# Performance work log

Hardware: AMD Instinct MI355X
Metric: run time of the kernel (lower is better)

Reference implementation:

```python
import jax, jax.numpy as jnp
import numpy as np

B, L = 8, 896
D_MODEL, N_HEAD, D_HEAD, D_INNER = 320, 10, 32, 1280
LN_EPS = 1e-5


def layernorm(x, g, b):
    mu = jnp.mean(x, axis=-1, keepdims=True)
    var = jnp.mean(jnp.square(x - mu), axis=-1, keepdims=True)
    return (x - mu) * jax.lax.rsqrt(var + LN_EPS) * g + b


def setup_inputs() -> dict:
    key = jax.random.key(0)
    ks = jax.random.split(key, 8)
    w = lambda k, shape: (jax.random.normal(k, shape, jnp.float32) * 0.02)
    return {
        "Z": jax.random.normal(ks[0], (B, L, D_MODEL), jnp.float32),
        "D": jax.random.uniform(ks[1], (B, L, L), jnp.float32),  # nonneg sq-distance bias
        "new_mask": jnp.zeros((B, L, L), jnp.float32),           # additive mask (0 = keep)
        "mask": jnp.ones((B, L, L), jnp.float32),                # multiplicative validity mask
        "gamma": jnp.ones((4, 4), jnp.float32),
        "w_qkv": w(ks[2], (D_MODEL, 3 * D_MODEL)),
        "b_qkv": jnp.zeros((3 * D_MODEL,), jnp.float32),
        "w_o": w(ks[3], (D_MODEL, D_MODEL)),
        "ln1_g": jnp.ones((D_MODEL,), jnp.float32),
        "ln1_b": jnp.zeros((D_MODEL,), jnp.float32),
        "ln2_g": jnp.ones((D_MODEL,), jnp.float32),
        "ln2_b": jnp.zeros((D_MODEL,), jnp.float32),
        "w1": w(ks[4], (D_MODEL, D_INNER)),
        "b1": jnp.zeros((D_INNER,), jnp.float32),
        "w2": w(ks[5], (D_INNER, D_MODEL)),
        "b2": jnp.zeros((D_MODEL,), jnp.float32),
        "N": 128, "M": 256, "P": 512,
    }


def reference(Z, D, new_mask, mask, gamma, w_qkv, b_qkv, w_o,
              ln1_g, ln1_b, ln2_g, ln2_b, w1, b1, w2, b2, N, M, P):
    bsz, n_elem, _ = Z.shape
    sqrtd = np.sqrt(D_HEAD).astype(np.float32)

    # per-pair type bias: segment ids 0=atom,1=bond,2=triplet (use_quad=False)
    seg = jnp.concatenate([
        jnp.zeros((N,), jnp.int32),
        jnp.ones((M,), jnp.int32),
        jnp.full((P,), 2, jnp.int32),
    ])  # [L]
    gamma_mask = gamma[seg[:, None], seg[None, :]]  # [L, L]

    inp = Z
    Zn = layernorm(Z, ln1_g, ln1_b)
    qkv = (Zn @ w_qkv + b_qkv).reshape(bsz, n_elem, N_HEAD, 3 * D_HEAD)
    Z2, Z3, Z4 = jnp.split(qkv, 3, axis=3)  # each [b, L, h, d]

    # scores [b, h, n, m]
    scores = jnp.einsum('bnhd,bmhd->bhnm', Z3, Z4) / sqrtd
    W = -(gamma_mask[None] * D)[:, None] + scores + new_mask[:, None]
    W = jax.nn.softmax(W, axis=3) * mask[:, None]

    attn_out = jnp.einsum('bhnm,bmhd->bnhd', W, Z2).reshape(bsz, n_elem, D_MODEL)
    attn_out = jax.nn.leaky_relu(attn_out, 0.01) @ w_o  # o_net has no bias
    Z_res = attn_out + inp

    Zn2 = layernorm(Z_res, ln2_g, ln2_b)
    out = jax.nn.relu(Zn2 @ w1 + b1) @ w2 + b2 + Z_res
    return out
```

## Files before the change

kernel.cpp:

```cpp
#include <hip/hip_runtime.h>

#define BB 8
#define LLEN 896
#define DMODEL 320
#define NHEAD 10
#define DHEAD 32
#define DINNER 1280
#define ROWS (BB*LLEN)

typedef float f32x4 __attribute__((ext_vector_type(4)));
typedef float f32x16 __attribute__((ext_vector_type(16)));
typedef __bf16 bf16x8 __attribute__((ext_vector_type(8)));

__device__ __forceinline__ float bf2f(unsigned short u) {
    union { unsigned int i; float f; } x;
    x.i = ((unsigned int)u) << 16;
    return x.f;
}
__device__ __forceinline__ unsigned short f2bf(float f) {
    unsigned int u = __float_as_uint(f);
    u += 0x7FFF + ((u >> 16) & 1);
    return (unsigned short)(u >> 16);
}

#define GLOAD16(g, l)                                                              \
    __builtin_amdgcn_global_load_lds(                                              \
        (const __attribute__((address_space(1))) void*)(g),                        \
        (__attribute__((address_space(3))) void*)(__attribute__((address_space(3))) char*)(l), \
        16, 0, 0)

__global__ __launch_bounds__(256) void prep_all(const float* __restrict__ w_qkv,
                                                const float* __restrict__ w_o,
                                                const float* __restrict__ w1,
                                                const float* __restrict__ w2,
                                                unsigned short* __restrict__ wqkvT,
                                                unsigned short* __restrict__ woT,
                                                unsigned short* __restrict__ w1T,
                                                unsigned short* __restrict__ w2T) {
    __shared__ float tile[32][33];
    int bid = blockIdx.x;
    const float* src; unsigned short* dst; int R, C, t;
    if (bid < 300)      { src = w_qkv; dst = wqkvT; R = 320;  C = 960;  t = bid; }
    else if (bid < 400) { src = w_o;   dst = woT;   R = 320;  C = 320;  t = bid - 300; }
    else if (bid < 800) { src = w1;    dst = w1T;   R = 320;  C = 1280; t = bid - 400; }
    else                { src = w2;    dst = w2T;   R = 1280; C = 320;  t = bid - 800; }
    int tiles_x = C >> 5;
    int c0 = (t % tiles_x) * 32;
    int r0 = (t / tiles_x) * 32;
    int tx = threadIdx.x & 31, ty = threadIdx.x >> 5;
#pragma unroll
    for (int k = 0; k < 4; ++k) {
        int yy = ty + 8 * k;
        tile[yy][tx] = src[(size_t)(r0 + yy) * C + c0 + tx];
    }
    __syncthreads();
#pragma unroll
    for (int k = 0; k < 4; ++k) {
        int yy = ty + 8 * k;
        dst[(size_t)(c0 + yy) * R + r0 + tx] = f2bf(tile[tx][yy]);
    }
}

__global__ __launch_bounds__(256) void prepass(const float* __restrict__ D,
                                               const float* __restrict__ nm,
                                               const float* __restrict__ mk,
                                               const float* __restrict__ gamma,
                                               unsigned int* __restrict__ combo) {
    __shared__ unsigned int tile[32][33];
    int mt = blockIdx.x, m0 = mt * 32;
    int n0 = blockIdx.y * 32;
    int b = blockIdx.z;
    int sn = (n0 < 128) ? 0 : (n0 < 384) ? 1 : 2;
    int sm = (m0 < 128) ? 0 : (m0 < 384) ? 1 : 2;
    float g = gamma[sn * 4 + sm];
    int tx = threadIdx.x & 31, ty = threadIdx.x >> 5;
#pragma unroll
    for (int k = 0; k < 4; ++k) {
        int nl = ty + 8 * k;
        size_t idx = ((size_t)b * LLEN + n0 + nl) * LLEN + m0 + tx;
        float bias = (-g * D[idx] + nm[idx]) * 1.4426950408889634f;
        tile[nl][tx] = (unsigned int)f2bf(bias) | ((unsigned int)f2bf(mk[idx]) << 16);
    }
    __syncthreads();
#pragma unroll
    for (int k = 0; k < 4; ++k) {
        int nl = ty + 8 * k;
        combo[(((size_t)b * 28 + mt) * LLEN + n0 + nl) * 32 + tx] = tile[nl][tx];
    }
}

__global__ __launch_bounds__(320) void ln_kernel(const float* __restrict__ x,
                                                 const float* __restrict__ g,
                                                 const float* __restrict__ bia,
                                                 unsigned short* __restrict__ y) {
    int row = blockIdx.x;
    int t = threadIdx.x;
    float v = x[(size_t)row * DMODEL + t];
    float s = v;
#pragma unroll
    for (int o = 1; o < 64; o <<= 1) s += __shfl_xor(s, o, 64);
    __shared__ float red[10];
    int w = t >> 6;
    if ((t & 63) == 0) red[w] = s;
    __syncthreads();
    float mu = (red[0] + red[1] + red[2] + red[3] + red[4]) * (1.0f / DMODEL);
    float d = v - mu;
    float s2 = d * d;
#pragma unroll
    for (int o = 1; o < 64; o <<= 1) s2 += __shfl_xor(s2, o, 64);
    if ((t & 63) == 0) red[5 + w] = s2;
    __syncthreads();
    float var = (red[5] + red[6] + red[7] + red[8] + red[9]) * (1.0f / DMODEL);
    float inv = rsqrtf(var + 1e-5f);
    y[(size_t)row * DMODEL + t] = f2bf(d * inv * g[t] + bia[t]);
}

template <int EPI>
__global__ __launch_bounds__(256) void gemm_bt(const unsigned short* __restrict__ A,
                                               const unsigned short* __restrict__ BT,
                                               const float* __restrict__ bias,
                                               const float* __restrict__ resid,
                                               void* __restrict__ outv,
                                               unsigned short* __restrict__ vtout,
                                               int M, int N, int K) {
    __shared__ unsigned short As[2][128][64];
    __shared__ unsigned short Bs[2][64][64];
    int tid = threadIdx.x;
    int m0 = blockIdx.x * 128;
    int n0 = blockIdx.y * 64;
    int wid = tid >> 6, l = tid & 63;
    int wr = wid >> 1, wc = wid & 1;
    int lr = l & 15, lh = l >> 4;
    int srow = tid >> 3;
    int sslot = (tid & 7) ^ (srow & 7);

    f32x4 acc[4][2];
#pragma unroll
    for (int mi = 0; mi < 4; ++mi)
#pragma unroll
        for (int ni = 0; ni < 2; ++ni) acc[mi][ni] = (f32x4){0.f, 0.f, 0.f, 0.f};

#define STAGE(buf, k0)                                                              \
    {                                                                               \
        _Pragma("unroll")                                                           \
        for (int i = 0; i < 4; ++i)                                                 \
            GLOAD16(&A[(size_t)(m0 + i * 32 + srow) * K + (k0) + sslot * 8],        \
                    (char*)&As[buf][0][0] + i * 4096 + tid * 16);                   \
        _Pragma("unroll")                                                           \
        for (int i = 0; i < 2; ++i)                                                 \
            GLOAD16(&BT[(size_t)(n0 + i * 32 + srow) * K + (k0) + sslot * 8],       \
                    (char*)&Bs[buf][0][0] + i * 4096 + tid * 16);                   \
    }

    int nsteps = K >> 6;
    STAGE(0, 0);
    int cur = 0;
#pragma unroll 1
    for (int t = 0; t < nsteps; ++t) {
        if (t + 1 < nsteps) {
            STAGE(cur ^ 1, (t + 1) * 64);
            asm volatile("s_waitcnt vmcnt(6)" ::: "memory");
        } else {
            asm volatile("s_waitcnt vmcnt(0)" ::: "memory");
        }
        __builtin_amdgcn_s_barrier();
#pragma unroll
        for (int kk = 0; kk < 2; ++kk) {
            int gch = kk * 4 + lh;
            int sl = gch ^ (lr & 7);
            bf16x8 b0 = *(const bf16x8*)&Bs[cur][wc * 32 + lr][sl * 8];
            bf16x8 b1 = *(const bf16x8*)&Bs[cur][wc * 32 + 16 + lr][sl * 8];
#pragma unroll
            for (int mi = 0; mi < 4; ++mi) {
                bf16x8 a = *(const bf16x8*)&As[cur][wr * 64 + mi * 16 + lr][sl * 8];
                acc[mi][0] = __builtin_amdgcn_mfma_f32_16x16x32_bf16(a, b0, acc[mi][0], 0, 0, 0);
                acc[mi][1] = __builtin_amdgcn_mfma_f32_16x16x32_bf16(a, b1, acc[mi][1], 0, 0, 0);
            }
        }
        __builtin_amdgcn_s_barrier();
        cur ^= 1;
    }
#undef STAGE

    unsigned short* outb = (unsigned short*)outv;
    float* outf = (float*)outv;
#pragma unroll
    for (int mi = 0; mi < 4; ++mi)
#pragma unroll
        for (int ni = 0; ni < 2; ++ni) {
            int col = n0 + wc * 32 + ni * 16 + lr;
            float bv = (EPI != 1) ? bias[col] : 0.f;
            unsigned short vv[4];
#pragma unroll
            for (int j = 0; j < 4; ++j) {
                int row = m0 + wr * 64 + mi * 16 + lh * 4 + j;
                float v = acc[mi][ni][j];
                if (EPI == 0 || EPI == 2 || EPI == 3) v += bv;
                if (EPI == 2) v = fmaxf(v, 0.0f);
                if (EPI == 1 || EPI == 3) v += resid[(size_t)row * N + col];
                if (EPI == 0 || EPI == 2) {
                    unsigned short ob = f2bf(v);
                    outb[(size_t)row * N + col] = ob;
                    vv[j] = ob;
                } else outf[(size_t)row * N + col] = v;
            }
            if (EPI == 0 && vtout) {
                int cf = n0 + wc * 32 + ni * 16;
                int h = cf / 96;
                int d0 = cf - h * 96;
                if (d0 < 32) {
                    int b2 = blockIdx.x / 7;
                    int mf = (blockIdx.x % 7) * 128 + wr * 64 + mi * 16 + lh * 4;
                    unsigned short* vp =
                        vtout + (((size_t)b2 * NHEAD + h) * 32 + d0 + lr) * LLEN + mf;
                    *(ushort4*)vp = *(ushort4*)vv;
                }
            }
        }
}

__global__ __launch_bounds__(320) void attn_mfma(const unsigned short* __restrict__ qkv,
                                                 const unsigned short* __restrict__ Vt,
                                                 const unsigned int* __restrict__ combo,
                                                 unsigned short* __restrict__ attn) {
    int tid = threadIdx.x;
    int h = blockIdx.x * 5 + (tid >> 6);
    int l = tid & 63;
    int c = l & 31;
    int hi = l >> 5;
    int nt = blockIdx.y % 28;
    int b = blockIdx.y / 28;
    int n0 = nt * 32;

    size_t qbase = ((size_t)(b * LLEN + n0 + c)) * 960 + h * 96 + 32 + hi * 8;
    bf16x8 qB0 = *(const bf16x8*)&qkv[qbase];
    bf16x8 qB1 = *(const bf16x8*)&qkv[qbase + 16];

    const unsigned int* cbase = combo + ((size_t)b * 28 * LLEN + n0 + c) * 32;
    size_t kbase = (size_t)b * LLEN * 960 + h * 96 + 64 + hi * 8;
    const unsigned short* vrow = Vt + (((size_t)b * NHEAD + h) * 32 + c) * LLEN;

#define ALOAD(mt, K0, K1, V1_, V2_, X4)                                     \
    {                                                                       \
        size_t krow = kbase + (size_t)((mt) * 32 + c) * 960;                \
        K0 = *(const bf16x8*)&qkv[krow];                                    \
        K1 = *(const bf16x8*)&qkv[krow + 16];                               \
        V1_ = *(const bf16x8*)&vrow[(mt) * 32 + hi * 8];                    \
        V2_ = *(const bf16x8*)&vrow[(mt) * 32 + 16 + hi * 8];               \
        const unsigned int* cp = cbase + (size_t)(mt) * (LLEN * 32);        \
        X4[0] = *(const int4*)&cp[4 * hi];                                  \
        X4[1] = *(const int4*)&cp[8 + 4 * hi];                              \
        X4[2] = *(const int4*)&cp[16 + 4 * hi];                             \
        X4[3] = *(const int4*)&cp[24 + 4 * hi];                             \
    }

#define ACOMPUTE(K0, K1, V1_, V2_, X4, OACC, LSUM)                                    \
    {                                                                                 \
        f32x16 sacc = {0.f,0.f,0.f,0.f,0.f,0.f,0.f,0.f,0.f,0.f,0.f,0.f,0.f,0.f,0.f,0.f}; \
        sacc = __builtin_amdgcn_mfma_f32_32x32x16_bf16(K0, qB0, sacc, 0, 0, 0);       \
        sacc = __builtin_amdgcn_mfma_f32_32x32x16_bf16(K1, qB1, sacc, 0, 0, 0);       \
        float p[16];                                                                  \
        _Pragma("unroll")                                                             \
        for (int r = 0; r < 16; ++r) {                                                \
            unsigned int cm = ((const unsigned int*)X4)[r];                           \
            float bias = __uint_as_float(cm << 16);                                   \
            float mk = __uint_as_float(cm & 0xffff0000u);                             \
            float e = exp2f(fmaf(sacc[r], 0.25500527f, bias));                        \
            LSUM += e;                                                                \
            p[r] = e * mk;                                                            \
        }                                                                             \
        unsigned int u[8], x[8];                                                      \
        _Pragma("unroll")                                                             \
        for (int j = 0; j < 8; ++j) {                                                 \
            asm("v_cvt_pk_bf16_f32 %0, %1, %2"                                        \
                : "=v"(u[j]) : "v"(p[2 * j]), "v"(p[2 * j + 1]));                     \
            x[j] = (unsigned int)__shfl_xor((int)u[j], 32, 64);                       \
        }                                                                             \
        union { unsigned int w[4]; bf16x8 v; } a1, a2;                                \
        if (hi == 0) {                                                                \
            a1.w[0] = u[0]; a1.w[1] = u[1]; a1.w[2] = x[0]; a1.w[3] = x[1];           \
            a2.w[0] = u[4]; a2.w[1] = u[5]; a2.w[2] = x[4]; a2.w[3] = x[5];           \
        } else {                                                                      \
            a1.w[0] = x[2]; a1.w[1] = x[3]; a1.w[2] = u[2]; a1.w[3] = u[3];           \
            a2.w[0] = x[6]; a2.w[1] = x[7]; a2.w[2] = u[6]; a2.w[3] = u[7];           \
        }                                                                             \
        OACC = __builtin_amdgcn_mfma_f32_32x32x16_bf16(a1.v, V1_, OACC, 0, 0, 0);     \
        OACC = __builtin_amdgcn_mfma_f32_32x32x16_bf16(a2.v, V2_, OACC, 0, 0, 0);     \
    }

    f32x16 oaccA = {0.f,0.f,0.f,0.f,0.f,0.f,0.f,0.f,0.f,0.f,0.f,0.f,0.f,0.f,0.f,0.f};
    f32x16 oaccB = oaccA;
    float lsumA = 0.f, lsumB = 0.f;
    bf16x8 k0A, k1A, v1A, v2A; int4 xA[4];
    bf16x8 k0B, k1B, v1B, v2B; int4 xB[4];
    ALOAD(0, k0A, k1A, v1A, v2A, xA);
    ALOAD(14, k0B, k1B, v1B, v2B, xB);
#pragma unroll 1
    for (int i = 0; i < 14; ++i) {
        ACOMPUTE(k0A, k1A, v1A, v2A, xA, oaccA, lsumA);
        if (i < 13) ALOAD(i + 1, k0A, k1A, v1A, v2A, xA);
        ACOMPUTE(k0B, k1B, v1B, v2B, xB, oaccB, lsumB);
        if (i < 13) ALOAD(i + 15, k0B, k1B, v1B, v2B, xB);
    }
#undef ALOAD
#undef ACOMPUTE

    f32x16 oacc = oaccA + oaccB;
    float lsum = lsumA + lsumB;
    lsum += __shfl_xor(lsum, 32, 64);
    float invs = 1.0f / lsum;
#pragma unroll
    for (int r = 0; r < 16; ++r) {
        int n = (r & 3) + 8 * (r >> 2) + 4 * hi;
        float o = oacc[r] * __shfl(invs, n, 64);
        o = (o >= 0.f) ? o : 0.01f * o;
        attn[((size_t)(b * LLEN + n0 + n)) * DMODEL + h * DHEAD + c] = f2bf(o);
    }
}

extern "C" void kernel_launch(void* const* d_in, const int* in_sizes, int n_in,
                              void* d_out, int out_size, void* d_ws, size_t ws_size,
                              hipStream_t stream) {
    const float* Z     = (const float*)d_in[0];
    const float* Dm    = (const float*)d_in[1];
    const float* nmask = (const float*)d_in[2];
    const float* mask  = (const float*)d_in[3];
    const float* gamma = (const float*)d_in[4];
    const float* w_qkv = (const float*)d_in[5];
    const float* b_qkv = (const float*)d_in[6];
    const float* w_o   = (const float*)d_in[7];
    const float* ln1g  = (const float*)d_in[8];
    const float* ln1b  = (const float*)d_in[9];
    const float* ln2g  = (const float*)d_in[10];
    const float* ln2b  = (const float*)d_in[11];
    const float* w1    = (const float*)d_in[12];
    const float* b1    = (const float*)d_in[13];
    const float* w2    = (const float*)d_in[14];
    const float* b2    = (const float*)d_in[15];

    char* ws = (char*)d_ws;
    unsigned short* Zn    = (unsigned short*)(ws + 0);
    unsigned short* qkv   = (unsigned short*)(ws + 4587520);
    unsigned short* attn  = (unsigned short*)(ws + 18350080);
    float*          Zres  = (float*)(ws + 22937600);
    unsigned short* Zn2   = (unsigned short*)(ws + 32112640);
    unsigned short* Hbuf  = (unsigned short*)(ws + 36700160);
    unsigned short* wqkvT = (unsigned short*)(ws + 55050240);
    unsigned short* woT   = (unsigned short*)(ws + 55664640);
    unsigned short* w1T   = (unsigned short*)(ws + 55869440);
    unsigned short* w2T   = (unsigned short*)(ws + 56688640);
    unsigned int*   combo = (unsigned int*)(ws + 57507840);
    unsigned short* Vtb   = (unsigned short*)(ws + 83197952);

    prep_all<<<1200, 256, 0, stream>>>(w_qkv, w_o, w1, w2, wqkvT, woT, w1T, w2T);

    prepass<<<dim3(28, 28, 8), 256, 0, stream>>>(Dm, nmask, mask, gamma, combo);

    ln_kernel<<<ROWS, 320, 0, stream>>>(Z, ln1g, ln1b, Zn);

    gemm_bt<0><<<dim3(ROWS / 128, 960 / 64), 256, 0, stream>>>(Zn, wqkvT, b_qkv, nullptr,
                                                               (void*)qkv, Vtb, ROWS, 960, 320);

    attn_mfma<<<dim3(2, BB * 28), 320, 0, stream>>>(qkv, Vtb, combo, attn);

    gemm_bt<1><<<dim3(ROWS / 128, 320 / 64), 256, 0, stream>>>(attn, woT, nullptr, Z,
                                                               (void*)Zres, nullptr, ROWS, 320, 320);

    ln_kernel<<<ROWS, 320, 0, stream>>>(Zres, ln2g, ln2b, Zn2);

    gemm_bt<2><<<dim3(ROWS / 128, 1280 / 64), 256, 0, stream>>>(Zn2, w1T, b1, nullptr,
                                                                (void*)Hbuf, nullptr, ROWS, 1280, 320);

    gemm_bt<3><<<dim3(ROWS / 128, 320 / 64), 256, 0, stream>>>(Hbuf, w2T, b2, Zres,
                                                               d_out, nullptr, ROWS, 320, 1280);
}
```

Measured before the change: 298.2 us.

## Use simple 64x64 GEMM tiles and split attention keys across two waves

Replaces the double-buffered async-to-LDS GEMM mainloop with a simple synchronous 64x64 tile that stages 32-wide K slices through padded shared memory. Attention now launches one head per block, with two waves splitting the key range and combining partial outputs and row sums through shared memory. The aim is more blocks and lower per-block resource use. In exchange it gives up load/compute overlap and per-tile data reuse in the GEMMs, and adds a barrier and an LDS reduction in attention.

```diff
diff --git a/kernel.cpp b/kernel.cpp
--- a/kernel.cpp
+++ b/kernel.cpp
@@ -22,12 +22,6 @@
     u += 0x7FFF + ((u >> 16) & 1);
     return (unsigned short)(u >> 16);
 }
-
-#define GLOAD16(g, l)                                                              \
-    __builtin_amdgcn_global_load_lds(                                              \
-        (const __attribute__((address_space(1))) void*)(g),                        \
-        (__attribute__((address_space(3))) void*)(__attribute__((address_space(3))) char*)(l), \
-        16, 0, 0)
 
 __global__ __launch_bounds__(256) void prep_all(const float* __restrict__ w_qkv,
                                                 const float* __restrict__ w_o,
@@ -123,78 +117,46 @@
                                                void* __restrict__ outv,
                                                unsigned short* __restrict__ vtout,
                                                int M, int N, int K) {
-    __shared__ unsigned short As[2][128][64];
-    __shared__ unsigned short Bs[2][64][64];
+    __shared__ unsigned short As[64][40];
+    __shared__ unsigned short Bs[64][40];
     int tid = threadIdx.x;
-    int m0 = blockIdx.x * 128;
+    int m0 = blockIdx.x * 64;
     int n0 = blockIdx.y * 64;
     int wid = tid >> 6, l = tid & 63;
     int wr = wid >> 1, wc = wid & 1;
+    int sr = tid >> 2, sc = (tid & 3) * 8;
     int lr = l & 15, lh = l >> 4;
-    int srow = tid >> 3;
-    int sslot = (tid & 7) ^ (srow & 7);
-
-    f32x4 acc[4][2];
-#pragma unroll
-    for (int mi = 0; mi < 4; ++mi)
-#pragma unroll
-        for (int ni = 0; ni < 2; ++ni) acc[mi][ni] = (f32x4){0.f, 0.f, 0.f, 0.f};
-
-#define STAGE(buf, k0)                                                              \
-    {                                                                               \
-        _Pragma("unroll")                                                           \
-        for (int i = 0; i < 4; ++i)                                                 \
-            GLOAD16(&A[(size_t)(m0 + i * 32 + srow) * K + (k0) + sslot * 8],        \
-                    (char*)&As[buf][0][0] + i * 4096 + tid * 16);                   \
-        _Pragma("unroll")                                                           \
-        for (int i = 0; i < 2; ++i)                                                 \
-            GLOAD16(&BT[(size_t)(n0 + i * 32 + srow) * K + (k0) + sslot * 8],       \
-                    (char*)&Bs[buf][0][0] + i * 4096 + tid * 16);                   \
-    }
-
-    int nsteps = K >> 6;
-    STAGE(0, 0);
-    int cur = 0;
-#pragma unroll 1
-    for (int t = 0; t < nsteps; ++t) {
-        if (t + 1 < nsteps) {
-            STAGE(cur ^ 1, (t + 1) * 64);
-            asm volatile("s_waitcnt vmcnt(6)" ::: "memory");
-        } else {
-            asm volatile("s_waitcnt vmcnt(0)" ::: "memory");
-        }
-        __builtin_amdgcn_s_barrier();
-#pragma unroll
-        for (int kk = 0; kk < 2; ++kk) {
-            int gch = kk * 4 + lh;
-            int sl = gch ^ (lr & 7);
-            bf16x8 b0 = *(const bf16x8*)&Bs[cur][wc * 32 + lr][sl * 8];
-            bf16x8 b1 = *(const bf16x8*)&Bs[cur][wc * 32 + 16 + lr][sl * 8];
-#pragma unroll
-            for (int mi = 0; mi < 4; ++mi) {
-                bf16x8 a = *(const bf16x8*)&As[cur][wr * 64 + mi * 16 + lr][sl * 8];
-                acc[mi][0] = __builtin_amdgcn_mfma_f32_16x16x32_bf16(a, b0, acc[mi][0], 0, 0, 0);
-                acc[mi][1] = __builtin_amdgcn_mfma_f32_16x16x32_bf16(a, b1, acc[mi][1], 0, 0, 0);
-            }
-        }
-        __builtin_amdgcn_s_barrier();
-        cur ^= 1;
-    }
-#undef STAGE
+    f32x4 acc00 = {0.f, 0.f, 0.f, 0.f}, acc01 = acc00, acc10 = acc00, acc11 = acc00;
+
+    for (int k0 = 0; k0 < K; k0 += 32) {
+        __syncthreads();
+        *(int4*)&As[sr][sc] = *(const int4*)&A[(size_t)(m0 + sr) * K + k0 + sc];
+        *(int4*)&Bs[sr][sc] = *(const int4*)&BT[(size_t)(n0 + sr) * K + k0 + sc];
+        __syncthreads();
+        bf16x8 a0 = *(const bf16x8*)&As[wr * 32 + lr][lh * 8];
+        bf16x8 a1 = *(const bf16x8*)&As[wr * 32 + 16 + lr][lh * 8];
+        bf16x8 b0 = *(const bf16x8*)&Bs[wc * 32 + lr][lh * 8];
+        bf16x8 b1 = *(const bf16x8*)&Bs[wc * 32 + 16 + lr][lh * 8];
+        acc00 = __builtin_amdgcn_mfma_f32_16x16x32_bf16(a0, b0, acc00, 0, 0, 0);
+        acc01 = __builtin_amdgcn_mfma_f32_16x16x32_bf16(a0, b1, acc01, 0, 0, 0);
+        acc10 = __builtin_amdgcn_mfma_f32_16x16x32_bf16(a1, b0, acc10, 0, 0, 0);
+        acc11 = __builtin_amdgcn_mfma_f32_16x16x32_bf16(a1, b1, acc11, 0, 0, 0);
+    }
 
     unsigned short* outb = (unsigned short*)outv;
     float* outf = (float*)outv;
 #pragma unroll
-    for (int mi = 0; mi < 4; ++mi)
+    for (int mi = 0; mi < 2; ++mi)
 #pragma unroll
         for (int ni = 0; ni < 2; ++ni) {
+            f32x4 a = (mi == 0) ? ((ni == 0) ? acc00 : acc01) : ((ni == 0) ? acc10 : acc11);
             int col = n0 + wc * 32 + ni * 16 + lr;
             float bv = (EPI != 1) ? bias[col] : 0.f;
             unsigned short vv[4];
 #pragma unroll
             for (int j = 0; j < 4; ++j) {
-                int row = m0 + wr * 64 + mi * 16 + lh * 4 + j;
-                float v = acc[mi][ni][j];
+                int row = m0 + wr * 32 + mi * 16 + lh * 4 + j;
+                float v = a[j];
                 if (EPI == 0 || EPI == 2 || EPI == 3) v += bv;
                 if (EPI == 2) v = fmaxf(v, 0.0f);
                 if (EPI == 1 || EPI == 3) v += resid[(size_t)row * N + col];
@@ -209,8 +171,8 @@
                 int h = cf / 96;
                 int d0 = cf - h * 96;
                 if (d0 < 32) {
-                    int b2 = blockIdx.x / 7;
-                    int mf = (blockIdx.x % 7) * 128 + wr * 64 + mi * 16 + lh * 4;
+                    int b2 = blockIdx.x / 14;
+                    int mf = (blockIdx.x % 14) * 64 + wr * 32 + mi * 16 + lh * 4;
                     unsigned short* vp =
                         vtout + (((size_t)b2 * NHEAD + h) * 32 + d0 + lr) * LLEN + mf;
                     *(ushort4*)vp = *(ushort4*)vv;
@@ -219,15 +181,16 @@
         }
 }
 
-__global__ __launch_bounds__(320) void attn_mfma(const unsigned short* __restrict__ qkv,
+__global__ __launch_bounds__(128) void attn_mfma(const unsigned short* __restrict__ qkv,
                                                  const unsigned short* __restrict__ Vt,
                                                  const unsigned int* __restrict__ combo,
                                                  unsigned short* __restrict__ attn) {
     int tid = threadIdx.x;
-    int h = blockIdx.x * 5 + (tid >> 6);
+    int w = tid >> 6;
     int l = tid & 63;
     int c = l & 31;
     int hi = l >> 5;
+    int h = blockIdx.x;
     int nt = blockIdx.y % 28;
     int b = blockIdx.y / 28;
     int n0 = nt * 32;
@@ -276,13 +239,13 @@
                 : "=v"(u[j]) : "v"(p[2 * j]), "v"(p[2 * j + 1]));                     \
             x[j] = (unsigned int)__shfl_xor((int)u[j], 32, 64);                       \
         }                                                                             \
-        union { unsigned int w[4]; bf16x8 v; } a1, a2;                                \
+        union { unsigned int ww[4]; bf16x8 v; } a1, a2;                               \
         if (hi == 0) {                                                                \
-            a1.w[0] = u[0]; a1.w[1] = u[1]; a1.w[2] = x[0]; a1.w[3] = x[1];           \
-            a2.w[0] = u[4]; a2.w[1] = u[5]; a2.w[2] = x[4]; a2.w[3] = x[5];           \
+            a1.ww[0] = u[0]; a1.ww[1] = u[1]; a1.ww[2] = x[0]; a1.ww[3] = x[1];       \
+            a2.ww[0] = u[4]; a2.ww[1] = u[5]; a2.ww[2] = x[4]; a2.ww[3] = x[5];       \
         } else {                                                                      \
-            a1.w[0] = x[2]; a1.w[1] = x[3]; a1.w[2] = u[2]; a1.w[3] = u[3];           \
-            a2.w[0] = x[6]; a2.w[1] = x[7]; a2.w[2] = u[6]; a2.w[3] = u[7];           \
+            a1.ww[0] = x[2]; a1.ww[1] = x[3]; a1.ww[2] = u[2]; a1.ww[3] = u[3];       \
+            a2.ww[0] = x[6]; a2.ww[1] = x[7]; a2.ww[2] = u[6]; a2.ww[3] = u[7];       \
         }                                                                             \
         OACC = __builtin_amdgcn_mfma_f32_32x32x16_bf16(a1.v, V1_, OACC, 0, 0, 0);     \
         OACC = __builtin_amdgcn_mfma_f32_32x32x16_bf16(a2.v, V2_, OACC, 0, 0, 0);     \
@@ -293,14 +256,15 @@
     float lsumA = 0.f, lsumB = 0.f;
     bf16x8 k0A, k1A, v1A, v2A; int4 xA[4];
     bf16x8 k0B, k1B, v1B, v2B; int4 xB[4];
-    ALOAD(0, k0A, k1A, v1A, v2A, xA);
-    ALOAD(14, k0B, k1B, v1B, v2B, xB);
+    int mb = w * 14;
+    ALOAD(mb, k0A, k1A, v1A, v2A, xA);
+    ALOAD(mb + 7, k0B, k1B, v1B, v2B, xB);
 #pragma unroll 1
-    for (int i = 0; i < 14; ++i) {
+    for (int i = 0; i < 7; ++i) {
         ACOMPUTE(k0A, k1A, v1A, v2A, xA, oaccA, lsumA);
-        if (i < 13) ALOAD(i + 1, k0A, k1A, v1A, v2A, xA);
+        if (i < 6) ALOAD(mb + i + 1, k0A, k1A, v1A, v2A, xA);
         ACOMPUTE(k0B, k1B, v1B, v2B, xB, oaccB, lsumB);
-        if (i < 13) ALOAD(i + 15, k0B, k1B, v1B, v2B, xB);
+        if (i < 6) ALOAD(mb + i + 8, k0B, k1B, v1B, v2B, xB);
     }
 #undef ALOAD
 #undef ACOMPUTE
@@ -308,13 +272,26 @@
     f32x16 oacc = oaccA + oaccB;
     float lsum = lsumA + lsumB;
     lsum += __shfl_xor(lsum, 32, 64);
-    float invs = 1.0f / lsum;
-#pragma unroll
-    for (int r = 0; r < 16; ++r) {
-        int n = (r & 3) + 8 * (r >> 2) + 4 * hi;
-        float o = oacc[r] * __shfl(invs, n, 64);
-        o = (o >= 0.f) ? o : 0.01f * o;
-        attn[((size_t)(b * LLEN + n0 + n)) * DMODEL + h * DHEAD + c] = f2bf(o);
+
+    __shared__ float comb[17][64];
+    if (w == 1) {
+#pragma unroll
+        for (int r = 0; r < 16; ++r) comb[r][l] = oacc[r];
+        comb[16][l] = lsum;
+    }
+    __syncthreads();
+    if (w == 0) {
+#pragma unroll
+        for (int r = 0; r < 16; ++r) oacc[r] += comb[r][l];
+        lsum += comb[16][l];
+        float invs = 1.0f / lsum;
+#pragma unroll
+        for (int r = 0; r < 16; ++r) {
+            int n = (r & 3) + 8 * (r >> 2) + 4 * hi;
+            float o = oacc[r] * __shfl(invs, n, 64);
+            o = (o >= 0.f) ? o : 0.01f * o;
+            attn[((size_t)(b * LLEN + n0 + n)) * DMODEL + h * DHEAD + c] = f2bf(o);
+        }
     }
 }
 
@@ -358,19 +335,19 @@
 
     ln_kernel<<<ROWS, 320, 0, stream>>>(Z, ln1g, ln1b, Zn);
 
-    gemm_bt<0><<<dim3(ROWS / 128, 960 / 64), 256, 0, stream>>>(Zn, wqkvT, b_qkv, nullptr,
-                                                               (void*)qkv, Vtb, ROWS, 960, 320);
-
-    attn_mfma<<<dim3(2, BB * 28), 320, 0, stream>>>(qkv, Vtb, combo, attn);
-
-    gemm_bt<1><<<dim3(ROWS / 128, 320 / 64), 256, 0, stream>>>(attn, woT, nullptr, Z,
-                                                               (void*)Zres, nullptr, ROWS, 320, 320);
+    gemm_bt<0><<<dim3(ROWS / 64, 960 / 64), 256, 0, stream>>>(Zn, wqkvT, b_qkv, nullptr,
+                                                              (void*)qkv, Vtb, ROWS, 960, 320);
+
+    attn_mfma<<<dim3(NHEAD, BB * 28), 128, 0, stream>>>(qkv, Vtb, combo, attn);
+
+    gemm_bt<1><<<dim3(ROWS / 64, 320 / 64), 256, 0, stream>>>(attn, woT, nullptr, Z,
+                                                              (void*)Zres, nullptr, ROWS, 320, 320);
 
     ln_kernel<<<ROWS, 320, 0, stream>>>(Zres, ln2g, ln2b, Zn2);
 
-    gemm_bt<2><<<dim3(ROWS / 128, 1280 / 64), 256, 0, stream>>>(Zn2, w1T, b1, nullptr,
-                                                                (void*)Hbuf, nullptr, ROWS, 1280, 320);
-
-    gemm_bt<3><<<dim3(ROWS / 128, 320 / 64), 256, 0, stream>>>(Hbuf, w2T, b2, Zres,
-                                                               d_out, nullptr, ROWS, 320, 1280);
-}
+    gemm_bt<2><<<dim3(ROWS / 64, 1280 / 64), 256, 0, stream>>>(Zn2, w1T, b1, nullptr,
+                                                               (void*)Hbuf, nullptr, ROWS, 1280, 320);
+
+    gemm_bt<3><<<dim3(ROWS / 64, 320 / 64), 256, 0, stream>>>(Hbuf, w2T, b2, Zres,
+                                                              d_out, nullptr, ROWS, 320, 1280);
+}
```

Measured after the change: 303.8 us. No clear change (+1.9%).
